# Performance work log

Hardware: AMD Instinct MI355X
Metric: run time of the kernel (lower is better)

The kernel has to match this reference:

```python
import jax, jax.numpy as jnp
import numpy as np
from jax import lax

T, B, D, H, L = 256, 64, 512, 1024, 2


def _lstm_params(key):
    k = 1.0 / np.sqrt(H)
    params = {}
    in_dims = [D] + [H] * (L - 1)
    for l in range(L):
        key, k1, k2, k3, k4 = jax.random.split(key, 5)
        params[f"W_ih{l}"] = jax.random.uniform(k1, (4 * H, in_dims[l]), jnp.float32, -k, k)
        params[f"W_hh{l}"] = jax.random.uniform(k2, (4 * H, H), jnp.float32, -k, k)
        params[f"b_ih{l}"] = jax.random.uniform(k3, (4 * H,), jnp.float32, -k, k)
        params[f"b_hh{l}"] = jax.random.uniform(k4, (4 * H,), jnp.float32, -k, k)
    return params


def setup_inputs() -> dict:
    key = jax.random.key(0)
    k_in, k_rst, k_p = jax.random.split(key, 3)
    inp = {
        "input": jax.random.normal(k_in, (T, B, D), jnp.float32),
        "reset": jax.random.randint(k_rst, (T, B), 0, 2, jnp.int32),
        "h0": jnp.zeros((B, L, H), jnp.float32),
        "c0": jnp.zeros((B, L, H), jnp.float32),
    }
    inp.update(_lstm_params(k_p))
    return inp


def _run(input, reset_f, h0, c0, Wi, Wh, bi, bh):
    # state: [L, B, H]
    h = jnp.transpose(h0, (1, 0, 2))
    c = jnp.transpose(c0, (1, 0, 2))

    def step(carry, xt):
        h, c = carry
        x_t, r_t = xt  # x_t: [B, D], r_t: [B]
        keep = (1.0 - r_t)[None, :, None]  # reset gate zeroes state where reset==1
        h = h * keep
        c = c * keep
        x = x_t
        hs, cs = [], []
        for l in range(L):
            # gate order in torch nn.LSTM: i, f, g, o
            gates = x @ Wi[l].T + bi[l] + h[l] @ Wh[l].T + bh[l]
            i_g, f_g, g_g, o_g = jnp.split(gates, 4, axis=-1)
            c_new = jax.nn.sigmoid(f_g) * c[l] + jax.nn.sigmoid(i_g) * jnp.tanh(g_g)
            h_new = jax.nn.sigmoid(o_g) * jnp.tanh(c_new)
            hs.append(h_new)
            cs.append(c_new)
            x = h_new
        return (jnp.stack(hs), jnp.stack(cs)), x

    (h, c), outputs = lax.scan(step, (h, c), (input, reset_f))
    # back to [B, L, H] as in the torch module's returned state
    return outputs, jnp.transpose(h, (1, 0, 2)), jnp.transpose(c, (1, 0, 2))


def reference(input, reset, h0, c0, W_ih0, W_hh0, b_ih0, b_hh0, W_ih1, W_hh1, b_ih1, b_hh1):
    reset_f = reset.astype(jnp.float32)
    Wi = [W_ih0, W_ih1]
    Wh = [W_hh0, W_hh1]
    bi = [b_ih0, b_ih1]
    bh = [b_hh0, b_hh1]
    outputs, hN, cN = _run(input, reset_f, h0, c0, Wi, Wh, bi, bh)
    return outputs, (hN, cN)
```

## Files before the change

kernel.cpp:

```cpp
#include <hip/hip_runtime.h>

typedef __bf16 bf16x8 __attribute__((ext_vector_type(8)));
typedef float f32x4 __attribute__((ext_vector_type(4)));
typedef unsigned u32x4 __attribute__((ext_vector_type(4)));
typedef unsigned short u16;

constexpr int T = 256, B = 64, D = 512, H = 1024;
constexpr int G4 = 4 * H;
constexpr int NBLK = 256;
constexpr int NTHR = 256;
constexpr int BS = 32;
constexpr int MT = 2;

__device__ __forceinline__ u16 f2bf(float f) {
  unsigned u = __builtin_bit_cast(unsigned, f);
  u += 0x7fffu + ((u >> 16) & 1u);
  return (u16)(u >> 16);
}

__device__ __forceinline__ f32x4 mfma16(bf16x8 a, bf16x8 b, f32x4 c) {
  return __builtin_amdgcn_mfma_f32_16x16x32_bf16(a, b, c, 0, 0, 0);
}

__device__ __forceinline__ float sigm(float x) { return 1.f / (1.f + expf(-x)); }

__device__ __forceinline__ int ldflag(const int* f, int i) {
  return __hip_atomic_load(&f[i], __ATOMIC_RELAXED, __HIP_MEMORY_SCOPE_AGENT);
}

__global__ void cvt_bf16(const float* __restrict__ src, u16* __restrict__ dst, int n4) {
  int i = blockIdx.x * blockDim.x + threadIdx.x;
  int st = gridDim.x * blockDim.x;
  for (; i < n4; i += st) {
    float4 v = reinterpret_cast<const float4*>(src)[i];
    ushort4 o;
    o.x = f2bf(v.x); o.y = f2bf(v.y); o.z = f2bf(v.z); o.w = f2bf(v.w);
    reinterpret_cast<ushort4*>(dst)[i] = o;
  }
}

__global__ void init_state(const float* __restrict__ h0,
                           u16* __restrict__ xs1, u16* __restrict__ h1buf,
                           const float* __restrict__ bih0, const float* __restrict__ bhh0,
                           const float* __restrict__ bih1, const float* __restrict__ bhh1,
                           float* __restrict__ bias0, float* __restrict__ bias1,
                           int* __restrict__ flags) {
  int i = blockIdx.x * blockDim.x + threadIdx.x;
  if (i < NBLK) flags[i] = 0;
  if (i < 2 * B * H) {
    int l = i / (B * H), rem = i % (B * H);
    int b = rem / H, k = rem % H;
    u16 v = f2bf(h0[(size_t)b * 2 * H + (size_t)l * H + k]);
    if (l == 0) xs1[(size_t)b * H + k] = v;
    else        h1buf[(size_t)b * H + k] = v;
  }
  if (i < G4) {
    bias0[i] = bih0[i] + bhh0[i];
    bias1[i] = bih1[i] + bhh1[i];
  }
}

template <int L>
__device__ __forceinline__ void run_layer(
    const u16* __restrict__ xin, const u16* __restrict__ wx, const u16* __restrict__ wh,
    const float* __restrict__ bias, u16* __restrict__ xs1, u16* __restrict__ h1b,
    const float* __restrict__ c0, const int* __restrict__ reset,
    float* __restrict__ out, int* __restrict__ flags, int half, int col0,
    f32x4* __restrict__ red, unsigned* __restrict__ rbits, float* __restrict__ lbias,
    const int s1mask, const int h1mask, const int full) {
  constexpr int KX   = L ? H : D;
  constexpr int NCX  = KX / 32;
  constexpr int NCXW = NCX / 4;
  constexpr int NHW  = (H / 32) / 4;
  constexpr int NCW  = NCXW + NHW;
  const size_t BH = (size_t)B * H;
  const size_t OUT_HN = (size_t)T * BH;
  const size_t OUT_CN = OUT_HN + 2 * BH;

  const int tid  = threadIdx.x;
  const int ks   = tid >> 6;
  const int lane = tid & 63;
  const int q    = lane >> 4;
  const int ln   = lane & 15;

  for (int t = tid; t < T; t += NTHR) {
    unsigned v = 0;
#pragma unroll 8
    for (int i = 0; i < 32; ++i)
      v |= (unsigned)(reset[t * B + half * BS + i] & 1) << i;
    rbits[t] = v;
  }
  if (tid < 64) lbias[tid] = bias[(tid >> 4) * H + col0 + (tid & 15)];

  u32x4 wreg[4][NCW];
#pragma unroll
  for (int g = 0; g < 4; ++g)
#pragma unroll
    for (int cc = 0; cc < NCW; ++cc) {
      const bool isx = cc < NCXW;
      const int c = isx ? ks * NCXW + cc : ks * NHW + (cc - NCXW);
      const u16* W = isx ? wx : wh;
      const int stride = isx ? KX : H;
      const int kk = c * 32 + q * 8;
      wreg[g][cc] = *reinterpret_cast<const u32x4*>(
          W + (size_t)(g * H + col0 + ln) * stride + kk);
    }
#pragma unroll
  for (int g = 0; g < 4; ++g)
#pragma unroll
    for (int cc = 0; cc < NCW; ++cc)
      asm volatile("" : "+a"(wreg[g][cc]));

  const int b0l = (tid >> 4) * 4;
  const int cl  = col0 + (tid & 15);
  float creg[4] = {0.f, 0.f, 0.f, 0.f};
  if (tid < 128)
#pragma unroll
    for (int r = 0; r < 4; ++r)
      creg[r] = c0[(size_t)(half * BS + b0l + r) * 2 * H + (size_t)L * H + cl];

  __syncthreads();
  float bval[4];
#pragma unroll
  for (int g = 0; g < 4; ++g) bval[g] = lbias[g * 16 + (tid & 15)];

  float hv[4] = {0.f, 0.f, 0.f, 0.f};

  for (int s = 0; s <= T; ++s) {
    const bool active = (L == 0) ? (s < T) : (s >= 1);
    const int t = (L == 0) ? s : s - 1;
    if (active) {
      if (full) {
        if (L == 1) {
          while (ldflag(flags, half * 64 + lane) < s) __builtin_amdgcn_s_sleep(1);
        }
      } else {
        for (;;) {
          int a = ldflag(flags, lane),       b = ldflag(flags, 64 + lane);
          int c = ldflag(flags, 128 + lane), d = ldflag(flags, 192 + lane);
          int m1 = a < b ? a : b, m2 = c < d ? c : d;
          if ((m1 < m2 ? m1 : m2) >= s) break;
          __builtin_amdgcn_s_sleep(1);
        }
        __builtin_amdgcn_fence(__ATOMIC_ACQUIRE, "agent");
      }

      f32x4 acc[4][MT];
#pragma unroll
      for (int g = 0; g < 4; ++g)
#pragma unroll
        for (int m = 0; m < MT; ++m) acc[g][m] = (f32x4){0.f, 0.f, 0.f, 0.f};

      const u16* xsrc = (L == 0) ? xin + (size_t)t * B * D
                                 : xs1 + (size_t)(s & s1mask) * BH;
#pragma unroll
      for (int cc = 0; cc < NCXW; ++cc) {
        const int kk = (ks * NCXW + cc) * 32 + q * 8;
        uint4 f[MT];
#pragma unroll
        for (int m = 0; m < MT; ++m)
          f[m] = *reinterpret_cast<const uint4*>(
              xsrc + (size_t)(half * BS + 16 * m + ln) * KX + kk);
#pragma unroll
        for (int g = 0; g < 4; ++g)
#pragma unroll
          for (int m = 0; m < MT; ++m)
            acc[g][m] = mfma16(__builtin_bit_cast(bf16x8, f[m]),
                               __builtin_bit_cast(bf16x8, wreg[g][cc]), acc[g][m]);
      }

      if (full) {
        const int gbase = L * 128 + half * 64;
        while (ldflag(flags, gbase + lane) < s) __builtin_amdgcn_s_sleep(1);
      }

      const unsigned rw = rbits[t];
      const int rz0 = (int)((rw >> ln) & 1u);
      const int rz1 = (int)((rw >> (16 + ln)) & 1u);
      const u16* hsrc = (L == 0) ? xs1 + (size_t)(s & s1mask) * BH
                                 : h1b + (size_t)(t & h1mask) * BH;
#pragma unroll
      for (int cc = 0; cc < NHW; ++cc) {
        const int kk = (ks * NHW + cc) * 32 + q * 8;
        uint4 f[MT];
        f[0] = *reinterpret_cast<const uint4*>(
            hsrc + (size_t)(half * BS + ln) * H + kk);
        f[1] = *reinterpret_cast<const uint4*>(
            hsrc + (size_t)(half * BS + 16 + ln) * H + kk);
        if (rz0) f[0] = make_uint4(0u, 0u, 0u, 0u);
        if (rz1) f[1] = make_uint4(0u, 0u, 0u, 0u);
#pragma unroll
        for (int g = 0; g < 4; ++g)
#pragma unroll
          for (int m = 0; m < MT; ++m)
            acc[g][m] = mfma16(__builtin_bit_cast(bf16x8, f[m]),
                               __builtin_bit_cast(bf16x8, wreg[g][NCXW + cc]), acc[g][m]);
      }

#pragma unroll
      for (int g = 0; g < 4; ++g)
#pragma unroll
        for (int m = 0; m < MT; ++m)
          red[(g * 4 + ks) * (MT * 64) + m * 64 + lane] = acc[g][m];
      __syncthreads();

      if (tid < 128) {
        f32x4 gate[4];
#pragma unroll
        for (int g = 0; g < 4; ++g) {
          f32x4 sum = red[(g * 4 + 0) * (MT * 64) + tid];
#pragma unroll
          for (int w = 1; w < 4; ++w) sum += red[(g * 4 + w) * (MT * 64) + tid];
          gate[g] = sum + (f32x4){bval[g], bval[g], bval[g], bval[g]};
        }
        const unsigned rstw = rbits[t] >> b0l;
        u16 hb[4];
#pragma unroll
        for (int r = 0; r < 4; ++r) {
          float cp = ((rstw >> r) & 1u) ? 0.f : creg[r];
          float i_ = sigm(gate[0][r]);
          float f_ = sigm(gate[1][r]);
          float g_ = tanhf(gate[2][r]);
          float o_ = sigm(gate[3][r]);
          float cn = fmaf(f_, cp, i_ * g_);
          float hn = o_ * tanhf(cn);
          creg[r] = cn;
          hv[r] = hn;
          hb[r] = f2bf(hn);
        }
        u16* hdst = (L == 0)
            ? xs1 + (size_t)((s + 1) & s1mask) * BH
            : h1b + (size_t)((t + 1) & h1mask) * BH;
#pragma unroll
        for (int r = 0; r < 4; ++r) {
          unsigned own = hb[r];
          unsigned oth = (unsigned)__shfl_xor((int)own, 1);
          unsigned pk = (tid & 1) ? ((oth & 0xffffu) | (own << 16))
                                  : (own | (oth << 16));
          if ((r >> 1) == (tid & 1))
            __hip_atomic_store(
                reinterpret_cast<unsigned*>(
                    hdst + (size_t)(half * BS + b0l + r) * H + (cl & ~1)),
                pk, __ATOMIC_RELAXED, __HIP_MEMORY_SCOPE_AGENT);
        }
        if (t == T - 1) {
#pragma unroll
          for (int r = 0; r < 4; ++r) {
            const size_t brow = (size_t)(half * BS + b0l + r);
            __builtin_nontemporal_store(
                hv[r], &out[OUT_HN + brow * 2 * H + (size_t)L * H + cl]);
            __builtin_nontemporal_store(
                creg[r], &out[OUT_CN + brow * 2 * H + (size_t)L * H + cl]);
            if (L == 1)
              __builtin_nontemporal_store(
                  hv[r], &out[(size_t)t * BH + brow * H + cl]);
          }
        }
      }
    }

    if (s < T) {
      __syncthreads();
      if (tid == 0)
        __hip_atomic_store(&flags[blockIdx.x], s + 1,
                           __ATOMIC_RELAXED, __HIP_MEMORY_SCOPE_AGENT);
      if (L == 1 && active && t < T - 1 && tid < 128) {
#pragma unroll
        for (int r = 0; r < 4; ++r)
          __builtin_nontemporal_store(
              hv[r], &out[(size_t)t * BH + (size_t)(half * BS + b0l + r) * H + cl]);
      }
    }
  }
}

__global__ void __launch_bounds__(NTHR, 1) lstm_seq(
    const u16* __restrict__ xin,
    const u16* __restrict__ wx0, const u16* __restrict__ wh0,
    const u16* __restrict__ wx1, const u16* __restrict__ wh1,
    const float* __restrict__ bias0, const float* __restrict__ bias1,
    u16* __restrict__ xs1, u16* __restrict__ h1b,
    const float* __restrict__ c0, const int* __restrict__ reset,
    float* __restrict__ out, int* __restrict__ flags,
    int s1mask, int h1mask, int full) {
  __shared__ f32x4 red[4 * 4 * MT * 64];
  __shared__ unsigned rbits[T];
  __shared__ float lbias[64];
  const int group = blockIdx.x >> 7;
  const int half  = (blockIdx.x >> 6) & 1;
  const int col0  = (blockIdx.x & 63) << 4;
  if (group == 0)
    run_layer<0>(xin, wx0, wh0, bias0, xs1, h1b, c0, reset, out, flags, half, col0,
                 red, rbits, lbias, s1mask, h1mask, full);
  else
    run_layer<1>(nullptr, wx1, wh1, bias1, xs1, h1b, c0, reset, out, flags, half, col0,
                 red, rbits, lbias, s1mask, h1mask, full);
}

extern "C" void kernel_launch(void* const* d_in, const int* in_sizes, int n_in,
                              void* d_out, int out_size, void* d_ws, size_t ws_size,
                              hipStream_t stream) {
  (void)in_sizes; (void)n_in; (void)out_size;
  const float* input = (const float*)d_in[0];
  const int*   reset = (const int*)d_in[1];
  const float* h0    = (const float*)d_in[2];
  const float* c0    = (const float*)d_in[3];
  const float* Wih0  = (const float*)d_in[4];
  const float* Whh0  = (const float*)d_in[5];
  const float* bih0  = (const float*)d_in[6];
  const float* bhh0  = (const float*)d_in[7];
  const float* Wih1  = (const float*)d_in[8];
  const float* Whh1  = (const float*)d_in[9];
  const float* bih1  = (const float*)d_in[10];
  const float* bhh1  = (const float*)d_in[11];
  float* out = (float*)d_out;
  char* ws = (char*)d_ws;

  const size_t SLOT = (size_t)B * H * 2;
  const size_t FIXED = (size_t)G4 * D * 2 + 3 * (size_t)G4 * H * 2
                     + (size_t)T * B * D * 2
                     + 2 * (size_t)G4 * 4 + 4096;
  const bool full = ws_size >= FIXED + 2 * (size_t)(T + 1) * SLOT + 65536;
  const int d0 = full ? (T + 1) : 4;
  const int d1 = full ? (T + 1) : 2;
  const int s1mask = full ? 511 : 3;
  const int h1mask = full ? 511 : 1;

  size_t off = 0;
  auto alloc = [&](size_t bytes) { size_t o = off; off += (bytes + 255) & ~(size_t)255; return o; };
  u16* wx0 = (u16*)(ws + alloc((size_t)G4 * D * 2));
  u16* wh0 = (u16*)(ws + alloc((size_t)G4 * H * 2));
  u16* wx1 = (u16*)(ws + alloc((size_t)G4 * H * 2));
  u16* wh1 = (u16*)(ws + alloc((size_t)G4 * H * 2));
  u16* xin = (u16*)(ws + alloc((size_t)T * B * D * 2));
  u16* xs1 = (u16*)(ws + alloc((size_t)d0 * SLOT));
  u16* h1b = (u16*)(ws + alloc((size_t)d1 * SLOT));
  float* pb0 = (float*)(ws + alloc((size_t)G4 * 4));
  float* pb1 = (float*)(ws + alloc((size_t)G4 * 4));
  int* flg = (int*)(ws + alloc(1024));

  cvt_bf16<<<1024, 256, 0, stream>>>(Wih0, wx0, G4 * D / 4);
  cvt_bf16<<<1024, 256, 0, stream>>>(Whh0, wh0, G4 * H / 4);
  cvt_bf16<<<1024, 256, 0, stream>>>(Wih1, wx1, G4 * H / 4);
  cvt_bf16<<<1024, 256, 0, stream>>>(Whh1, wh1, G4 * H / 4);
  cvt_bf16<<<2048, 256, 0, stream>>>(input, xin, T * B * D / 4);
  init_state<<<512, 256, 0, stream>>>(h0, xs1, h1b, bih0, bhh0, bih1, bhh1, pb0, pb1, flg);
  lstm_seq<<<NBLK, NTHR, 0, stream>>>(xin, wx0, wh0, wx1, wh1, pb0, pb1,
                                      xs1, h1b, c0, reset, out, flg,
                                      s1mask, h1mask, full ? 1 : 0);
}
```

Baseline: 2.079 ms.

## Prefetch next-step input fragments after flag publish and hoist h loads

In the full (group-split) mode, the input-projection fragments for step s+1 are now loaded right after this block publishes its step flag. For layer 1 this first waits on the layer-0 flag for s+1, which moves the x-side load latency off the recurrent critical path. The hidden-state fragments are all loaded up front after the recurrent flag wait, before any MFMA, instead of being interleaved per chunk. The cost is more live registers for the xf and hf arrays, and an extra early wait on layer-0 flags in the layer-1 blocks.

After: 1.955 ms. 6.0% less time.

```diff
diff --git a/kernel.cpp b/kernel.cpp
--- a/kernel.cpp
+++ b/kernel.cpp
@@ -126,14 +126,27 @@
 
   float hv[4] = {0.f, 0.f, 0.f, 0.f};
 
+  uint4 xf[NCXW][MT];
+  auto load_xfrags = [&](const u16* xsrc) {
+#pragma unroll
+    for (int cc = 0; cc < NCXW; ++cc) {
+      const int kk = (ks * NCXW + cc) * 32 + q * 8;
+#pragma unroll
+      for (int m = 0; m < MT; ++m)
+        xf[cc][m] = *reinterpret_cast<const uint4*>(
+            xsrc + (size_t)(half * BS + 16 * m + ln) * KX + kk);
+    }
+  };
+  if (full && L == 0) load_xfrags(xin);
+
   for (int s = 0; s <= T; ++s) {
     const bool active = (L == 0) ? (s < T) : (s >= 1);
     const int t = (L == 0) ? s : s - 1;
     if (active) {
       if (full) {
-        if (L == 1) {
-          while (ldflag(flags, half * 64 + lane) < s) __builtin_amdgcn_s_sleep(1);
-        }
+        const int gbase = L * 128 + half * 64;
+        while (ldflag(flags, gbase + lane) < s) __builtin_amdgcn_s_sleep(1);
+        asm volatile("" ::: "memory");
       } else {
         for (;;) {
           int a = ldflag(flags, lane),       b = ldflag(flags, 64 + lane);
@@ -143,6 +156,22 @@
           __builtin_amdgcn_s_sleep(1);
         }
         __builtin_amdgcn_fence(__ATOMIC_ACQUIRE, "agent");
+        asm volatile("" ::: "memory");
+        const u16* xsrc = (L == 0) ? xin + (size_t)t * B * D
+                                   : xs1 + (size_t)(s & s1mask) * BH;
+        load_xfrags(xsrc);
+      }
+
+      const u16* hsrc = (L == 0) ? xs1 + (size_t)(s & s1mask) * BH
+                                 : h1b + (size_t)(t & h1mask) * BH;
+      uint4 hf[NHW][MT];
+#pragma unroll
+      for (int cc = 0; cc < NHW; ++cc) {
+        const int kk = (ks * NHW + cc) * 32 + q * 8;
+#pragma unroll
+        for (int m = 0; m < MT; ++m)
+          hf[cc][m] = *reinterpret_cast<const uint4*>(
+              hsrc + (size_t)(half * BS + 16 * m + ln) * H + kk);
       }
 
       f32x4 acc[4][MT];
@@ -151,50 +180,30 @@
 #pragma unroll
         for (int m = 0; m < MT; ++m) acc[g][m] = (f32x4){0.f, 0.f, 0.f, 0.f};
 
-      const u16* xsrc = (L == 0) ? xin + (size_t)t * B * D
-                                 : xs1 + (size_t)(s & s1mask) * BH;
-#pragma unroll
-      for (int cc = 0; cc < NCXW; ++cc) {
-        const int kk = (ks * NCXW + cc) * 32 + q * 8;
-        uint4 f[MT];
-#pragma unroll
-        for (int m = 0; m < MT; ++m)
-          f[m] = *reinterpret_cast<const uint4*>(
-              xsrc + (size_t)(half * BS + 16 * m + ln) * KX + kk);
+#pragma unroll
+      for (int cc = 0; cc < NCXW; ++cc)
 #pragma unroll
         for (int g = 0; g < 4; ++g)
 #pragma unroll
           for (int m = 0; m < MT; ++m)
-            acc[g][m] = mfma16(__builtin_bit_cast(bf16x8, f[m]),
+            acc[g][m] = mfma16(__builtin_bit_cast(bf16x8, xf[cc][m]),
                                __builtin_bit_cast(bf16x8, wreg[g][cc]), acc[g][m]);
-      }
-
-      if (full) {
-        const int gbase = L * 128 + half * 64;
-        while (ldflag(flags, gbase + lane) < s) __builtin_amdgcn_s_sleep(1);
-      }
 
       const unsigned rw = rbits[t];
       const int rz0 = (int)((rw >> ln) & 1u);
       const int rz1 = (int)((rw >> (16 + ln)) & 1u);
-      const u16* hsrc = (L == 0) ? xs1 + (size_t)(s & s1mask) * BH
-                                 : h1b + (size_t)(t & h1mask) * BH;
+      const uint4 zz = make_uint4(0u, 0u, 0u, 0u);
 #pragma unroll
       for (int cc = 0; cc < NHW; ++cc) {
-        const int kk = (ks * NHW + cc) * 32 + q * 8;
-        uint4 f[MT];
-        f[0] = *reinterpret_cast<const uint4*>(
-            hsrc + (size_t)(half * BS + ln) * H + kk);
-        f[1] = *reinterpret_cast<const uint4*>(
-            hsrc + (size_t)(half * BS + 16 + ln) * H + kk);
-        if (rz0) f[0] = make_uint4(0u, 0u, 0u, 0u);
-        if (rz1) f[1] = make_uint4(0u, 0u, 0u, 0u);
-#pragma unroll
-        for (int g = 0; g < 4; ++g)
-#pragma unroll
-          for (int m = 0; m < MT; ++m)
-            acc[g][m] = mfma16(__builtin_bit_cast(bf16x8, f[m]),
-                               __builtin_bit_cast(bf16x8, wreg[g][NCXW + cc]), acc[g][m]);
+        const uint4 v0 = rz0 ? zz : hf[cc][0];
+        const uint4 v1 = rz1 ? zz : hf[cc][1];
+#pragma unroll
+        for (int g = 0; g < 4; ++g) {
+          acc[g][0] = mfma16(__builtin_bit_cast(bf16x8, v0),
+                             __builtin_bit_cast(bf16x8, wreg[g][NCXW + cc]), acc[g][0]);
+          acc[g][1] = mfma16(__builtin_bit_cast(bf16x8, v1),
+                             __builtin_bit_cast(bf16x8, wreg[g][NCXW + cc]), acc[g][1]);
+        }
       }
 
 #pragma unroll
@@ -269,6 +278,15 @@
         for (int r = 0; r < 4; ++r)
           __builtin_nontemporal_store(
               hv[r], &out[(size_t)t * BH + (size_t)(half * BS + b0l + r) * H + cl]);
+      }
+      if (full) {
+        if (L == 0) {
+          if (s + 1 < T) load_xfrags(xin + (size_t)(s + 1) * B * D);
+        } else {
+          while (ldflag(flags, half * 64 + lane) < s + 1) __builtin_amdgcn_s_sleep(1);
+          asm volatile("" ::: "memory");
+          load_xfrags(xs1 + (size_t)((s + 1) & s1mask) * BH);
+        }
       }
     }
   }
```
